# Kernel tuning notes

Measured on AMD Instinct MI355X. Metric: run time of the kernel, lower is better.

Reference implementation:

```python
import jax, jax.numpy as jnp
import numpy as np

# quantization formats
E_Q, M_Q = 4, 3      # E4M3 fp8 for input/param quantizers
E_A, M_A = 5, 10     # fp16-like accumulate / output format


def quant(x, exp, man):
    """Round-to-nearest-even float quantization to (exp, man) bits,
    with subnormals and saturation (mptorch float_quantize semantics)."""
    ebias = 2 ** (exp - 1) - 1
    emin = 1 - ebias                      # min normal exponent
    maxv = (2.0 - 2.0 ** (-man)) * 2.0 ** ebias
    ax = jnp.abs(x)
    e = jnp.floor(jnp.log2(jnp.where(ax > 0, ax, 1.0)))
    e = jnp.maximum(e, emin)              # subnormal range shares emin scale
    scale = jnp.exp2(man - e)
    q = jnp.round(x * scale) / scale      # jnp.round is half-to-even
    return jnp.clip(q, -maxv, maxv)


def qgemm(x, wt, exp_add, man_add):
    """Custom-precision GEMM x[M,K] @ wt[K,N] with fma=True:
    the running accumulator is requantized to (exp_add, man_add)
    after every rank-1 (per-k) fused multiply-add."""
    M, K = x.shape
    N = wt.shape[1]

    def step(acc, xw):
        xk, wk = xw                       # [M], [N]
        acc = quant(acc + xk[:, None] * wk[None, :], exp_add, man_add)
        return acc, None

    acc0 = jnp.zeros((M, N), x.dtype)
    acc, _ = jax.lax.scan(step, acc0, (x.T, wt))
    return acc


def setup_inputs() -> dict:
    key = jax.random.key(0)
    k1, k2, k3 = jax.random.split(key, 3)
    in_f, out_f, m = 1024, 1024, 2048
    x = jax.random.normal(k1, (m, in_f), jnp.float32)
    weight = jax.random.normal(k2, (out_f, in_f), jnp.float32) / np.float32(np.sqrt(in_f))
    bound = 1.0 / np.float32(np.sqrt(in_f))
    bias = jax.random.uniform(k3, (out_f,), jnp.float32, -bound, bound)
    return {"x": x, "weight": weight, "bias": bias}


def reference(x, weight, bias):
    qx = quant(x, E_Q, M_Q)               # input_quant
    qw = quant(weight, E_Q, M_Q)          # param_quant
    qb = quant(bias, E_Q, M_Q)            # param_quant
    out = qgemm(qx, qw.T, E_A, M_A)       # float_gemm with fma accumulation
    out = out + qb[None, :]
    out = quant(out, E_A, M_A)            # output requantization
    return out
```

## Files before the change

### kernel.cpp

```cpp
#include <hip/hip_runtime.h>
#include <hip/hip_fp16.h>


#define M_DIM 2048
#define N_DIM 1024
#define K_DIM 1024

#define BM 32
#define BN 128
#define BK 64

__device__ __forceinline__ float quant_e4m3(float v) {
  unsigned au = __float_as_uint(v) & 0x7fffffffu;
  if (au == 0u) return v;
  int e = (int)(au >> 23) - 127;
  if (e < -6) e = -6;
  float s  = __uint_as_float((unsigned)(130 - e) << 23);
  float is = __uint_as_float((unsigned)(124 + e) << 23);
  float r = rintf(v * s) * is;
  return fminf(240.f, fmaxf(-240.f, r));
}

__global__ __launch_bounds__(256) void qt_kernel(const float* __restrict__ in,
                                                 __half* __restrict__ outp,
                                                 int R, int C) {
  __shared__ float tile[32][33];
  const int tx = threadIdx.x & 31;
  const int ty = threadIdx.x >> 5;
  const int c0 = blockIdx.x * 32;
  const int r0 = blockIdx.y * 32;
#pragma unroll
  for (int i = 0; i < 4; i++) {
    int r = r0 + ty + i * 8;
    tile[ty + i * 8][tx] = quant_e4m3(in[(size_t)r * C + c0 + tx]);
  }
  __syncthreads();
#pragma unroll
  for (int i = 0; i < 4; i++) {
    int c = c0 + ty + i * 8;
    outp[(size_t)c * R + r0 + tx] = __float2half(tile[tx][ty + i * 8]);
  }
}

__global__ __launch_bounds__(256) void qbias_kernel(const float* __restrict__ b,
                                                    float* __restrict__ qb) {
  int i = blockIdx.x * 256 + threadIdx.x;
  qb[i] = quant_e4m3(b[i]);
}

__global__ __launch_bounds__(256, 2) void gemm_qfma(const __half* __restrict__ xT,
                                                    const __half* __restrict__ wT,
                                                    const float* __restrict__ qb,
                                                    float* __restrict__ outp) {
  __shared__ unsigned xs[BK][BM];
  __shared__ unsigned wsh[BK][BN / 2];
  const int tid = threadIdx.x;
  const int tn = tid & 31;
  const int tm = tid >> 5;
  const int bn0 = blockIdx.x * BN;
  const int bm0 = blockIdx.y * BM;

  __half2 acc[4][2];
#pragma unroll
  for (int i = 0; i < 4; i++)
#pragma unroll
    for (int j = 0; j < 2; j++) acc[i][j] = __float2half2_rn(0.0f);

  const int xr = tid >> 2;
  const int xc = (tid & 3) << 3;
  const int wc = (tid & 15) << 3;
  const int wr = tid >> 4;

  for (int kc = 0; kc < K_DIM; kc += BK) {
    __syncthreads();
    {
      uint4 v = *reinterpret_cast<const uint4*>(xT + (size_t)(kc + xr) * M_DIM + bm0 + xc);
      unsigned* d = &xs[xr][xc];
      d[0] = (v.x & 0xffffu) * 0x10001u;
      d[1] = (v.x >> 16)     * 0x10001u;
      d[2] = (v.y & 0xffffu) * 0x10001u;
      d[3] = (v.y >> 16)     * 0x10001u;
      d[4] = (v.z & 0xffffu) * 0x10001u;
      d[5] = (v.z >> 16)     * 0x10001u;
      d[6] = (v.w & 0xffffu) * 0x10001u;
      d[7] = (v.w >> 16)     * 0x10001u;
    }
#pragma unroll
    for (int p = 0; p < 4; p++) {
      const int r = wr + (p << 4);
      *reinterpret_cast<uint4*>(&wsh[r][wc >> 1]) =
          *reinterpret_cast<const uint4*>(wT + (size_t)(kc + r) * N_DIM + bn0 + wc);
    }
    __syncthreads();
#pragma unroll
    for (int kk = 0; kk < BK; kk++) {
      const uint4 xv = *reinterpret_cast<const uint4*>(&xs[kk][tm << 2]);
      const uint2 wv = *reinterpret_cast<const uint2*>(&wsh[kk][tn << 1]);
      const __half2 w0 = *reinterpret_cast<const __half2*>(&wv.x);
      const __half2 w1 = *reinterpret_cast<const __half2*>(&wv.y);
      const __half2 x0 = *reinterpret_cast<const __half2*>(&xv.x);
      const __half2 x1 = *reinterpret_cast<const __half2*>(&xv.y);
      const __half2 x2 = *reinterpret_cast<const __half2*>(&xv.z);
      const __half2 x3 = *reinterpret_cast<const __half2*>(&xv.w);
      acc[0][0] = __hfma2(x0, w0, acc[0][0]);
      acc[0][1] = __hfma2(x0, w1, acc[0][1]);
      acc[1][0] = __hfma2(x1, w0, acc[1][0]);
      acc[1][1] = __hfma2(x1, w1, acc[1][1]);
      acc[2][0] = __hfma2(x2, w0, acc[2][0]);
      acc[2][1] = __hfma2(x2, w1, acc[2][1]);
      acc[3][0] = __hfma2(x3, w0, acc[3][0]);
      acc[3][1] = __hfma2(x3, w1, acc[3][1]);
    }
  }

  const float4 bv = *reinterpret_cast<const float4*>(qb + bn0 + (tn << 2));
#pragma unroll
  for (int i = 0; i < 4; i++) {
    float4 o;
    o.x = __half2float(__float2half(__low2float(acc[i][0])  + bv.x));
    o.y = __half2float(__float2half(__high2float(acc[i][0]) + bv.y));
    o.z = __half2float(__float2half(__low2float(acc[i][1])  + bv.z));
    o.w = __half2float(__float2half(__high2float(acc[i][1]) + bv.w));
    *reinterpret_cast<float4*>(outp + (size_t)(bm0 + (tm << 2) + i) * N_DIM + bn0 + (tn << 2)) = o;
  }
}

extern "C" void kernel_launch(void* const* d_in, const int* in_sizes, int n_in,
                              void* d_out, int out_size, void* d_ws, size_t ws_size,
                              hipStream_t stream) {
  const float* x = (const float*)d_in[0];
  const float* w = (const float*)d_in[1];
  const float* b = (const float*)d_in[2];
  float* outp = (float*)d_out;

  char* ws = (char*)d_ws;
  __half* xT = (__half*)ws;
  __half* wT = (__half*)(ws + (size_t)(4 << 20));
  float*  qb = (float*)(ws + (size_t)(6 << 20));

  hipLaunchKernelGGL(qt_kernel, dim3(K_DIM / 32, M_DIM / 32), dim3(256), 0, stream,
                     x, xT, M_DIM, K_DIM);
  hipLaunchKernelGGL(qt_kernel, dim3(K_DIM / 32, N_DIM / 32), dim3(256), 0, stream,
                     w, wT, N_DIM, K_DIM);
  hipLaunchKernelGGL(qbias_kernel, dim3(N_DIM / 256), dim3(256), 0, stream, b, qb);
  hipLaunchKernelGGL(gemm_qfma, dim3(N_DIM / BN, M_DIM / BM), dim3(256), 0, stream,
                     xT, wT, qb, outp);
}
```

Before: 119.9 us.

## Double-buffer GEMM with direct global-to-LDS loads and op_sel packed FMAs

Rewrites the GEMM as a double-buffered pipeline that uses global_load_lds to move tiles straight into shared memory, so the loads for the next chunk overlap compute on the current one. X is now packed as k-pairs of halves, so the inner loop selects the lo or hi half through v_pk_fma_f16 op_sel instead of broadcasting at LDS store time. Each thread now computes an 8x4 output tile with 128 threads per block. Bias quantization is folded into the GEMM epilogue, which removes one launch. The risks are higher register pressure and per-thread work, plus correctness of the inline asm op_sel encoding. The k-order of the sequential fp16 accumulation is preserved.

```diff
diff --git a/kernel.cpp b/kernel.cpp
--- a/kernel.cpp
+++ b/kernel.cpp
@@ -9,6 +9,9 @@
 #define BM 32
 #define BN 128
 #define BK 64
+#define NCHUNK (K_DIM / BK)
+
+typedef unsigned u32;
 
 __device__ __forceinline__ float quant_e4m3(float v) {
   unsigned au = __float_as_uint(v) & 0x7fffffffu;
@@ -20,6 +23,7 @@
   float r = rintf(v * s) * is;
   return fminf(240.f, fmaxf(-240.f, r));
 }
+
 
 __global__ __launch_bounds__(256) void qt_kernel(const float* __restrict__ in,
                                                  __half* __restrict__ outp,
@@ -42,86 +46,128 @@
   }
 }
 
-__global__ __launch_bounds__(256) void qbias_kernel(const float* __restrict__ b,
-                                                    float* __restrict__ qb) {
-  int i = blockIdx.x * 256 + threadIdx.x;
-  qb[i] = quant_e4m3(b[i]);
+__global__ __launch_bounds__(256) void qt_pack_kernel(const float* __restrict__ in,
+                                                      u32* __restrict__ outp,
+                                                      int R, int C) {
+  __shared__ float tile[32][33];
+  const int tx = threadIdx.x & 31;
+  const int ty = threadIdx.x >> 5;
+  const int c0 = blockIdx.x * 32;
+  const int r0 = blockIdx.y * 32;
+#pragma unroll
+  for (int i = 0; i < 4; i++) {
+    int r = r0 + ty + i * 8;
+    tile[ty + i * 8][tx] = quant_e4m3(in[(size_t)r * C + c0 + tx]);
+  }
+  __syncthreads();
+#pragma unroll
+  for (int i = 0; i < 2; i++) {
+    int tl = ty + i * 8;
+    u32 lo = (u32)__half_as_ushort(__float2half(tile[tx][2 * tl]));
+    u32 hi = (u32)__half_as_ushort(__float2half(tile[tx][2 * tl + 1]));
+    outp[(size_t)(c0 / 2 + tl) * R + r0 + tx] = lo | (hi << 16);
+  }
 }
 
-__global__ __launch_bounds__(256, 2) void gemm_qfma(const __half* __restrict__ xT,
-                                                    const __half* __restrict__ wT,
-                                                    const float* __restrict__ qb,
-                                                    float* __restrict__ outp) {
-  __shared__ unsigned xs[BK][BM];
-  __shared__ unsigned wsh[BK][BN / 2];
+
+__device__ __forceinline__ void gld16(const void* g, void* l) {
+  __builtin_amdgcn_global_load_lds((const __attribute__((address_space(1))) u32*)g,
+                                   (__attribute__((address_space(3))) u32*)l, 16, 0, 0);
+}
+
+__device__ __forceinline__ void pkfma_lo(u32& acc, u32 x, u32 w) {
+  asm("v_pk_fma_f16 %0, %1, %2, %0 op_sel:[0,0,0] op_sel_hi:[0,1,1]"
+      : "+v"(acc) : "v"(x), "v"(w));
+}
+__device__ __forceinline__ void pkfma_hi(u32& acc, u32 x, u32 w) {
+  asm("v_pk_fma_f16 %0, %1, %2, %0 op_sel:[1,0,0] op_sel_hi:[1,1,1]"
+      : "+v"(acc) : "v"(x), "v"(w));
+}
+
+__global__ __launch_bounds__(128) void gemm_qfma(const u32* __restrict__ xP,
+                                                 const __half* __restrict__ wT,
+                                                 const float* __restrict__ b,
+                                                 float* __restrict__ outp) {
+  __shared__ __align__(16) u32 xs[2][BK / 2][BM];
+  __shared__ __align__(16) __half wsh[2][BK][BN];
   const int tid = threadIdx.x;
   const int tn = tid & 31;
   const int tm = tid >> 5;
   const int bn0 = blockIdx.x * BN;
   const int bm0 = blockIdx.y * BM;
+  const int xoff = tm << 3;
+  const int woff = tn << 2;
 
-  __half2 acc[4][2];
+  u32 acc[8][2];
 #pragma unroll
-  for (int i = 0; i < 4; i++)
+  for (int i = 0; i < 8; i++) { acc[i][0] = 0u; acc[i][1] = 0u; }
+
+  const __half* wsrc = wT + (size_t)(tid >> 4) * N_DIM + bn0 + ((tid & 15) << 3);
+  const u32*   xsrc = xP + (size_t)(tid >> 3) * M_DIM + bm0 + ((tid & 7) << 2);
+
+  auto stage = [&](int ch, int buf) {
+    const __half* wp = wsrc + (size_t)ch * BK * N_DIM;
+    char* wl = (char*)&wsh[buf][0][0] + tid * 16;
 #pragma unroll
-    for (int j = 0; j < 2; j++) acc[i][j] = __float2half2_rn(0.0f);
+    for (int j = 0; j < 8; j++)
+      gld16(wp + (size_t)(j * 8) * N_DIM, wl + j * 2048);
+    const u32* xp = xsrc + (size_t)ch * (BK / 2) * M_DIM;
+    char* xl = (char*)&xs[buf][0][0] + tid * 16;
+#pragma unroll
+    for (int j = 0; j < 2; j++)
+      gld16(xp + (size_t)(j * 16) * M_DIM, xl + j * 2048);
+  };
 
-  const int xr = tid >> 2;
-  const int xc = (tid & 3) << 3;
-  const int wc = (tid & 15) << 3;
-  const int wr = tid >> 4;
+  auto compute = [&](int buf) {
+#pragma unroll
+    for (int tp = 0; tp < BK / 2; tp++) {
+      u32 xv[8];
+      *reinterpret_cast<uint4*>(&xv[0]) =
+          *reinterpret_cast<const uint4*>(&xs[buf][tp][xoff]);
+      *reinterpret_cast<uint4*>(&xv[4]) =
+          *reinterpret_cast<const uint4*>(&xs[buf][tp][xoff + 4]);
+      const uint2 w0 = *reinterpret_cast<const uint2*>(&wsh[buf][2 * tp][woff]);
+      const uint2 w1 = *reinterpret_cast<const uint2*>(&wsh[buf][2 * tp + 1][woff]);
+#pragma unroll
+      for (int i = 0; i < 8; i++) {
+        pkfma_lo(acc[i][0], xv[i], w0.x);
+        pkfma_lo(acc[i][1], xv[i], w0.y);
+      }
+#pragma unroll
+      for (int i = 0; i < 8; i++) {
+        pkfma_hi(acc[i][0], xv[i], w1.x);
+        pkfma_hi(acc[i][1], xv[i], w1.y);
+      }
+    }
+  };
 
-  for (int kc = 0; kc < K_DIM; kc += BK) {
+  stage(0, 0);
+  __syncthreads();
+#pragma unroll 1
+  for (int ch = 0; ch < NCHUNK; ch += 2) {
+    stage(ch + 1, 1);
+    compute(0);
     __syncthreads();
-    {
-      uint4 v = *reinterpret_cast<const uint4*>(xT + (size_t)(kc + xr) * M_DIM + bm0 + xc);
-      unsigned* d = &xs[xr][xc];
-      d[0] = (v.x & 0xffffu) * 0x10001u;
-      d[1] = (v.x >> 16)     * 0x10001u;
-      d[2] = (v.y & 0xffffu) * 0x10001u;
-      d[3] = (v.y >> 16)     * 0x10001u;
-      d[4] = (v.z & 0xffffu) * 0x10001u;
-      d[5] = (v.z >> 16)     * 0x10001u;
-      d[6] = (v.w & 0xffffu) * 0x10001u;
-      d[7] = (v.w >> 16)     * 0x10001u;
-    }
-#pragma unroll
-    for (int p = 0; p < 4; p++) {
-      const int r = wr + (p << 4);
-      *reinterpret_cast<uint4*>(&wsh[r][wc >> 1]) =
-          *reinterpret_cast<const uint4*>(wT + (size_t)(kc + r) * N_DIM + bn0 + wc);
-    }
+    if (ch + 2 < NCHUNK) stage(ch + 2, 0);
+    compute(1);
     __syncthreads();
-#pragma unroll
-    for (int kk = 0; kk < BK; kk++) {
-      const uint4 xv = *reinterpret_cast<const uint4*>(&xs[kk][tm << 2]);
-      const uint2 wv = *reinterpret_cast<const uint2*>(&wsh[kk][tn << 1]);
-      const __half2 w0 = *reinterpret_cast<const __half2*>(&wv.x);
-      const __half2 w1 = *reinterpret_cast<const __half2*>(&wv.y);
-      const __half2 x0 = *reinterpret_cast<const __half2*>(&xv.x);
-      const __half2 x1 = *reinterpret_cast<const __half2*>(&xv.y);
-      const __half2 x2 = *reinterpret_cast<const __half2*>(&xv.z);
-      const __half2 x3 = *reinterpret_cast<const __half2*>(&xv.w);
-      acc[0][0] = __hfma2(x0, w0, acc[0][0]);
-      acc[0][1] = __hfma2(x0, w1, acc[0][1]);
-      acc[1][0] = __hfma2(x1, w0, acc[1][0]);
-      acc[1][1] = __hfma2(x1, w1, acc[1][1]);
-      acc[2][0] = __hfma2(x2, w0, acc[2][0]);
-      acc[2][1] = __hfma2(x2, w1, acc[2][1]);
-      acc[3][0] = __hfma2(x3, w0, acc[3][0]);
-      acc[3][1] = __hfma2(x3, w1, acc[3][1]);
-    }
   }
 
-  const float4 bv = *reinterpret_cast<const float4*>(qb + bn0 + (tn << 2));
+  float4 bq;
+  bq.x = quant_e4m3(b[bn0 + woff + 0]);
+  bq.y = quant_e4m3(b[bn0 + woff + 1]);
+  bq.z = quant_e4m3(b[bn0 + woff + 2]);
+  bq.w = quant_e4m3(b[bn0 + woff + 3]);
 #pragma unroll
-  for (int i = 0; i < 4; i++) {
+  for (int i = 0; i < 8; i++) {
+    __half2 a0 = *reinterpret_cast<__half2*>(&acc[i][0]);
+    __half2 a1 = *reinterpret_cast<__half2*>(&acc[i][1]);
     float4 o;
-    o.x = __half2float(__float2half(__low2float(acc[i][0])  + bv.x));
-    o.y = __half2float(__float2half(__high2float(acc[i][0]) + bv.y));
-    o.z = __half2float(__float2half(__low2float(acc[i][1])  + bv.z));
-    o.w = __half2float(__float2half(__high2float(acc[i][1]) + bv.w));
-    *reinterpret_cast<float4*>(outp + (size_t)(bm0 + (tm << 2) + i) * N_DIM + bn0 + (tn << 2)) = o;
+    o.x = __half2float(__float2half(__low2float(a0)  + bq.x));
+    o.y = __half2float(__float2half(__high2float(a0) + bq.y));
+    o.z = __half2float(__float2half(__low2float(a1)  + bq.z));
+    o.w = __half2float(__float2half(__high2float(a1) + bq.w));
+    *reinterpret_cast<float4*>(outp + (size_t)(bm0 + xoff + i) * N_DIM + bn0 + woff) = o;
   }
 }
 
@@ -134,15 +180,13 @@
   float* outp = (float*)d_out;
 
   char* ws = (char*)d_ws;
-  __half* xT = (__half*)ws;
+  u32*    xP = (u32*)ws;
   __half* wT = (__half*)(ws + (size_t)(4 << 20));
-  float*  qb = (float*)(ws + (size_t)(6 << 20));
 
-  hipLaunchKernelGGL(qt_kernel, dim3(K_DIM / 32, M_DIM / 32), dim3(256), 0, stream,
-                     x, xT, M_DIM, K_DIM);
+  hipLaunchKernelGGL(qt_pack_kernel, dim3(K_DIM / 32, M_DIM / 32), dim3(256), 0, stream,
+                     x, xP, M_DIM, K_DIM);
   hipLaunchKernelGGL(qt_kernel, dim3(K_DIM / 32, N_DIM / 32), dim3(256), 0, stream,
                      w, wT, N_DIM, K_DIM);
-  hipLaunchKernelGGL(qbias_kernel, dim3(N_DIM / 256), dim3(256), 0, stream, b, qb);
-  hipLaunchKernelGGL(gemm_qfma, dim3(N_DIM / BN, M_DIM / BM), dim3(256), 0, stream,
-                     xT, wT, qb, outp);
+  hipLaunchKernelGGL(gemm_qfma, dim3(N_DIM / BN, M_DIM / BM), dim3(128), 0, stream,
+                     xP, wT, b, outp);
 }
```

Result: slower. 151.2 us (+26.1%).
